# Performance work log

Measured on AMD Instinct MI355X. Metric: run time of the kernel, lower is better.

Reference implementation:

```python
import jax, jax.numpy as jnp
import numpy as np

D = 256
H = 8
DH = D // H
N = 100000
B = 256
T = 131072
HID_FUSE = 256   # fuse MLP hidden = d_model
HID_HEAD = 256   # QuantileHeads hidden
NQ = 3           # quantiles (q10, q50, q90)


def setup_inputs() -> dict:
    key = jax.random.key(0)
    ks = jax.random.split(key, 32)
    p = lambda k, *s: (0.02 * jax.random.normal(k, s, dtype=jnp.float32))
    inp = {
        'node_embeddings': jax.random.normal(ks[0], (N, D), dtype=jnp.float32),
        'target_index': jax.random.randint(ks[1], (B,), 0, N),
        'port_index': jax.random.randint(ks[2], (T,), 0, N),
        'port_batch': jnp.sort(jax.random.randint(ks[3], (T,), 0, B)),
        'port_weight': jax.random.uniform(ks[4], (T,), dtype=jnp.float32),
        # PMA pooling params (learnable seed + MHA projections, no biases)
        'seed': p(ks[5], D),
        'Wq_p': p(ks[6], D, D), 'Wk_p': p(ks[7], D, D), 'Wv_p': p(ks[8], D, D), 'Wo_p': p(ks[9], D, D),
        # target->portfolio cross-attention params
        'Wq_c': p(ks[10], D, D), 'Wk_c': p(ks[11], D, D), 'Wv_c': p(ks[12], D, D), 'Wo_c': p(ks[13], D, D),
        # fuse LayerNorm(3d) + MLP
        'ln_g': jnp.ones((3 * D,), jnp.float32), 'ln_b': jnp.zeros((3 * D,), jnp.float32),
        'fuse_W1': p(ks[14], 3 * D, HID_FUSE), 'fuse_b1': jnp.zeros((HID_FUSE,), jnp.float32),
        'fuse_W2': p(ks[15], HID_FUSE, D), 'fuse_b2': jnp.zeros((D,), jnp.float32),
        # quantile heads MLP
        'head_W1': p(ks[16], D, HID_HEAD), 'head_b1': jnp.zeros((HID_HEAD,), jnp.float32),
        'head_W2': p(ks[17], HID_HEAD, NQ), 'head_b2': jnp.zeros((NQ,), jnp.float32),
    }
    return inp


def _segment_attend(logits, v, seg, num_segments):
    # logits [T,H], v [T,H,DH], seg [T] -> pooled [num_segments, H, DH]
    m = jax.ops.segment_max(logits, seg, num_segments=num_segments)  # [B,H]
    e = jnp.exp(logits - m[seg])                                      # [T,H]
    s = jax.ops.segment_sum(e, seg, num_segments=num_segments)        # [B,H]
    p = e / (s[seg] + 1e-9)
    return jax.ops.segment_sum(p[..., None] * v, seg, num_segments=num_segments)


def reference(node_embeddings, target_index, port_index, port_batch, port_weight,
              seed, Wq_p, Wk_p, Wv_p, Wo_p, Wq_c, Wk_c, Wv_c, Wo_c,
              ln_g, ln_b, fuse_W1, fuse_b1, fuse_W2, fuse_b2,
              head_W1, head_b1, head_W2, head_b2):
    b = target_index.shape[0]
    scale = float(DH) ** -0.5
    tgt = node_embeddings[target_index]          # [B,D]
    tok = node_embeddings[port_index]            # [T,D]
    logw = jnp.log(port_weight + 1e-8)           # DV01 weighting as logit bias

    # --- PMA: learnable seed query pools DV01-weighted portfolio tokens ---
    q_p = (seed @ Wq_p).reshape(H, DH)
    k_p = (tok @ Wk_p).reshape(-1, H, DH)
    v_p = (tok @ Wv_p).reshape(-1, H, DH)
    lg_p = jnp.einsum('thd,hd->th', k_p, q_p) * scale + logw[:, None]
    pooled = _segment_attend(lg_p, v_p, port_batch, b).reshape(b, D)
    contexts = pooled @ Wo_p                     # [B,D]; zeros for empty portfolios

    # --- target -> portfolio cross-attention (residual) ---
    q_c = (tgt @ Wq_c).reshape(b, H, DH)
    k_c = (tok @ Wk_c).reshape(-1, H, DH)
    v_c = (tok @ Wv_c).reshape(-1, H, DH)
    lg_c = jnp.einsum('thd,thd->th', k_c, q_c[port_batch]) * scale + logw[:, None]
    att = _segment_attend(lg_c, v_c, port_batch, b).reshape(b, D)
    fused = tgt + att @ Wo_c                     # [B,D]; == tgt for empty portfolios

    # --- fuse: concat -> LN -> MLP ---
    z = jnp.concatenate([tgt, contexts, fused], axis=-1)  # [B,3D]
    mu = jnp.mean(z, axis=-1, keepdims=True)
    var = jnp.var(z, axis=-1, keepdims=True)
    z = (z - mu) * jax.lax.rsqrt(var + 1e-5) * ln_g + ln_b
    z = jax.nn.relu(z @ fuse_W1 + fuse_b1) @ fuse_W2 + fuse_b2  # [B,D]

    # --- quantile heads ---
    out = jax.nn.relu(z @ head_W1 + head_b1) @ head_W2 + head_b2  # [B,NQ]
    return out
```

## Files before the change

### kernel.cpp

```cpp
#include <hip/hip_runtime.h>
#include <hip/hip_bf16.h>

typedef __attribute__((ext_vector_type(8))) short short8;
typedef __attribute__((ext_vector_type(4))) float floatx4;

#define SCALE 0.17677669529663687f

__device__ __forceinline__ unsigned short f2bf(float f) {
  unsigned int x = __float_as_uint(f);
  x += 0x7fffu + ((x >> 16) & 1u);
  return (unsigned short)(x >> 16);
}
__device__ __forceinline__ float bf2f(unsigned short u) {
  return __uint_as_float(((unsigned int)u) << 16);
}

__device__ __forceinline__ short8 load_cvt8(const float* p) {
  floatx4 a = *(const floatx4*)p;
  floatx4 b = *(const floatx4*)(p + 4);
  short8 r;
  r[0] = (short)f2bf(a[0]); r[1] = (short)f2bf(a[1]);
  r[2] = (short)f2bf(a[2]); r[3] = (short)f2bf(a[3]);
  r[4] = (short)f2bf(b[0]); r[5] = (short)f2bf(b[1]);
  r[6] = (short)f2bf(b[2]); r[7] = (short)f2bf(b[3]);
  return r;
}

__device__ __forceinline__ void matvec256(const float* __restrict__ W,
                                          const float* act, float* outv,
                                          float* red4, int tid) {
  const int c4 = tid & 63, kg = tid >> 6, c0 = c4 * 4;
  floatx4 acc = (floatx4){0.f, 0.f, 0.f, 0.f};
  const float* Wp = W + (size_t)(kg * 64) * 256 + c0;
  const float* ap = act + kg * 64;
  #pragma unroll 8
  for (int k = 0; k < 64; ++k) {
    floatx4 wv = *(const floatx4*)(Wp + (size_t)k * 256);
    float a = ap[k];
    acc[0] += a * wv[0]; acc[1] += a * wv[1];
    acc[2] += a * wv[2]; acc[3] += a * wv[3];
  }
  *(floatx4*)(red4 + kg * 256 + c0) = acc;
  __syncthreads();
  outv[tid] = red4[tid] + red4[256 + tid] + red4[512 + tid] + red4[768 + tid];
  __syncthreads();
}

__global__ __launch_bounds__(256) void setup_kernel(
    const float* __restrict__ node,
    const int* __restrict__ tgt_idx,
    const int* __restrict__ port_batch,
    const float* __restrict__ seed,
    const float* __restrict__ Wq_p,
    const float* __restrict__ Wk_p,
    const float* __restrict__ Wq_c,
    const float* __restrict__ Wk_c,
    unsigned short* __restrict__ u_p_t,
    unsigned short* __restrict__ u_c_all,
    int* __restrict__ seg, int T, int B)
{
  __shared__ float act_l[256];
  __shared__ float q_l[256];
  __shared__ __align__(16) float red4[1024];
  const int tid = threadIdx.x;
  const int b = blockIdx.x;

  if (tid == 0 || (tid == 64 && b == B - 1)) {
    int key = (tid == 0) ? b : B;
    int lo = 0, hi = T;
    while (lo < hi) { int mid = (lo + hi) >> 1; if (port_batch[mid] < key) lo = mid + 1; else hi = mid; }
    seg[key] = lo;
  }

  act_l[tid] = node[(size_t)tgt_idx[b] * 256 + tid];
  __syncthreads();
  matvec256(Wq_c, act_l, q_l, red4, tid);

  {
    float hs[8];
    #pragma unroll
    for (int h = 0; h < 8; ++h) hs[h] = 0.f;
    #pragma unroll
    for (int c = 0; c < 32; ++c) {
      floatx4 wa = *(const floatx4*)(Wk_c + (size_t)tid * 256 + c * 8);
      floatx4 wb = *(const floatx4*)(Wk_c + (size_t)tid * 256 + c * 8 + 4);
      const int h = c >> 2;
      #pragma unroll
      for (int j = 0; j < 4; ++j) hs[h] += wa[j] * q_l[c * 8 + j];
      #pragma unroll
      for (int j = 0; j < 4; ++j) hs[h] += wb[j] * q_l[c * 8 + 4 + j];
    }
    #pragma unroll
    for (int h = 0; h < 8; ++h)
      u_c_all[(size_t)b * 2048 + h * 256 + tid] = f2bf(hs[h]);
  }

  if (b == 0) {
    __syncthreads();
    act_l[tid] = seed[tid];
    __syncthreads();
    matvec256(Wq_p, act_l, q_l, red4, tid);
    float hs[8];
    #pragma unroll
    for (int h = 0; h < 8; ++h) hs[h] = 0.f;
    #pragma unroll
    for (int c = 0; c < 32; ++c) {
      floatx4 wa = *(const floatx4*)(Wk_p + (size_t)tid * 256 + c * 8);
      floatx4 wb = *(const floatx4*)(Wk_p + (size_t)tid * 256 + c * 8 + 4);
      const int h = c >> 2;
      #pragma unroll
      for (int j = 0; j < 4; ++j) hs[h] += wa[j] * q_l[c * 8 + j];
      #pragma unroll
      for (int j = 0; j < 4; ++j) hs[h] += wb[j] * q_l[c * 8 + 4 + j];
    }
    #pragma unroll
    for (int h = 0; h < 8; ++h) u_p_t[h * 256 + tid] = f2bf(hs[h]);
  }
}

__global__ __launch_bounds__(256, 4) void attn_kernel(
    const float* __restrict__ node,
    const int* __restrict__ port_index,
    const float* __restrict__ port_weight,
    const unsigned short* __restrict__ u_p_t,
    const unsigned short* __restrict__ u_c_all,
    const int* __restrict__ seg,
    float* __restrict__ slabs, int T, int S)
{
  __shared__ __align__(16) unsigned short tok_lds[64 * 264];
  __shared__ __align__(16) unsigned short E_t[16 * 72];
  __shared__ float l_lds[16];

  const int tid  = threadIdx.x;
  const int s    = blockIdx.x;
  const int b    = blockIdx.y;
  const int lane = tid & 63;
  const int w    = tid >> 6;
  const int q    = lane >> 4;
  const int n    = lane & 15;

  if (tid < 16) l_lds[tid] = 0.f;

  short8 ufrag[8];
  const unsigned short* ubase = (n < 8) ? (u_p_t + n * 256)
                                        : (u_c_all + (size_t)b * 2048 + (n - 8) * 256);
  #pragma unroll
  for (int s8 = 0; s8 < 8; ++s8)
    ufrag[s8] = *(const short8*)(ubase + q * 8 + s8 * 32);

  const int start  = seg[b];
  const int end    = seg[b + 1];
  const int ntiles = (end - start + 63) >> 6;

  floatx4 sacc[4];
  #pragma unroll
  for (int nt = 0; nt < 4; ++nt) sacc[nt] = (floatx4){0.f, 0.f, 0.f, 0.f};

  short8 cur[8], nxt[8];
  float pwc[4], pwn[4];

  __syncthreads();

  if (s < ntiles) {
    int t = start + s * 64 + w * 16 + n; int tc = t < T ? t : T - 1;
    const float* rp = node + (size_t)port_index[tc] * 256 + q * 8;
    #pragma unroll
    for (int k = 0; k < 8; ++k) cur[k] = load_cvt8(rp + k * 32);
    #pragma unroll
    for (int r = 0; r < 4; ++r) { int tr = start + s * 64 + w * 16 + q * 4 + r; pwc[r] = port_weight[tr < T ? tr : T - 1]; }
  }

  for (int it = s; it < ntiles; it += S) {
    const int tbase = start + it * 64;
    if (it + S < ntiles) {
      int t = start + (it + S) * 64 + w * 16 + n; int tc = t < T ? t : T - 1;
      const float* rp = node + (size_t)port_index[tc] * 256 + q * 8;
      #pragma unroll
      for (int k = 0; k < 8; ++k) nxt[k] = load_cvt8(rp + k * 32);
      #pragma unroll
      for (int r = 0; r < 4; ++r) { int tr = start + (it + S) * 64 + w * 16 + q * 4 + r; pwn[r] = port_weight[tr < T ? tr : T - 1]; }
    }
    floatx4 lacc = (floatx4){0.f, 0.f, 0.f, 0.f};
    #pragma unroll
    for (int k = 0; k < 8; ++k)
      lacc = __builtin_amdgcn_mfma_f32_16x16x32_bf16(cur[k], ufrag[k], lacc, 0, 0, 0);
    float lsum = 0.f;
    #pragma unroll
    for (int r = 0; r < 4; ++r) {
      const int tr = tbase + w * 16 + q * 4 + r;
      float e = 0.f;
      if (tr < end) {
        float lg = lacc[r] * SCALE + logf(pwc[r] + 1e-8f);
        e = __expf(lg);
      }
      unsigned short eb = f2bf(e);
      E_t[n * 72 + w * 16 + q * 4 + r] = eb;
      lsum += bf2f(eb);
    }
    lsum += __shfl_xor(lsum, 16, 64);
    lsum += __shfl_xor(lsum, 32, 64);
    if (lane < 16) atomicAdd(&l_lds[lane], lsum);
    #pragma unroll
    for (int k = 0; k < 8; ++k)
      *(short8*)(tok_lds + (w * 16 + n) * 264 + q * 8 + k * 32) = cur[k];
    __syncthreads();
    short8 ea0 = *(const short8*)(E_t + n * 72 + q * 8);
    short8 ea1 = *(const short8*)(E_t + n * 72 + 32 + q * 8);
    #pragma unroll
    for (int nt = 0; nt < 4; ++nt) {
      const int dcol = w * 64 + nt * 16 + n;
      short8 b0, b1;
      #pragma unroll
      for (int j = 0; j < 8; ++j) b0[j] = (short)tok_lds[(q * 8 + j) * 264 + dcol];
      #pragma unroll
      for (int j = 0; j < 8; ++j) b1[j] = (short)tok_lds[(32 + q * 8 + j) * 264 + dcol];
      sacc[nt] = __builtin_amdgcn_mfma_f32_16x16x32_bf16(ea0, b0, sacc[nt], 0, 0, 0);
      sacc[nt] = __builtin_amdgcn_mfma_f32_16x16x32_bf16(ea1, b1, sacc[nt], 0, 0, 0);
    }
    __syncthreads();
    #pragma unroll
    for (int k = 0; k < 8; ++k) cur[k] = nxt[k];
    #pragma unroll
    for (int r = 0; r < 4; ++r) pwc[r] = pwn[r];
  }

  float* sl = slabs + ((size_t)b * S + s) * 4224;
  #pragma unroll
  for (int nt = 0; nt < 4; ++nt)
    #pragma unroll
    for (int r = 0; r < 4; ++r)
      sl[(q * 4 + r) * 256 + w * 64 + nt * 16 + n] = sacc[nt][r];
  if (tid < 16) sl[4096 + tid] = l_lds[tid];
}

__global__ __launch_bounds__(256) void k_slab_gemm(
    const float* __restrict__ slabs, int S,
    const float* __restrict__ Wv_p, const float* __restrict__ Wv_c,
    float* __restrict__ X)
{
  __shared__ float act_l[4 * 256];
  __shared__ float lsum[4];
  const int tid = threadIdx.x;
  const int bt = blockIdx.x, nt = blockIdx.y, z = blockIdx.z;
  const int head = nt >> 1;
  const int row = z * 8 + head;
  if (tid < 4) {
    const float* sl = slabs + (size_t)(bt * 4 + tid) * S * 4224;
    float l = 0.f;
    for (int s = 0; s < S; ++s) l += sl[s * 4224 + 4096 + row];
    lsum[tid] = 1.0f / (l + 1e-9f);
  }
  __syncthreads();
  for (int i = tid; i < 4 * 256; i += 256) {
    int m = i >> 8, k = i & 255;
    const float* sl = slabs + (size_t)(bt * 4 + m) * S * 4224;
    float sum = 0.f;
    for (int s = 0; s < S; ++s) sum += sl[s * 4224 + row * 256 + k];
    act_l[i] = sum * lsum[m];
  }
  __syncthreads();
  const int m = tid >> 6, lane = tid & 63, ks = lane >> 4, n = lane & 15;
  const int n0 = nt * 16;
  const float* W = z ? Wv_c : Wv_p;
  float acc = 0.f;
  const float* Wp = W + (size_t)(ks * 64) * 256 + n0 + n;
  const float* ap = &act_l[m * 256 + ks * 64];
  #pragma unroll 8
  for (int k = 0; k < 64; ++k) acc += ap[k] * Wp[(size_t)k * 256];
  acc += __shfl_xor(acc, 16, 64);
  acc += __shfl_xor(acc, 32, 64);
  if (ks == 0)
    X[(size_t)(bt * 4 + m) * 512 + z * 256 + n0 + n] = acc;
}

__global__ __launch_bounds__(256) void k_plain_gemm(
    const float* __restrict__ act, int act_ld,
    const float* __restrict__ W0, const float* __restrict__ W1,
    const float* __restrict__ bias0, const float* __restrict__ bias1,
    float* __restrict__ outp, int out_ld,
    int K, int relu)
{
  __shared__ float act_l[4 * 768];
  const int tid = threadIdx.x;
  const int bt = blockIdx.x, nt = blockIdx.y, z = blockIdx.z;
  const float* W = z ? W1 : W0;
  const float* bias = z ? bias1 : bias0;
  for (int i = tid; i < 4 * K; i += 256) {
    int m = i / K, k = i - m * K;
    act_l[m * K + k] = act[(size_t)(bt * 4 + m) * act_ld + z * K + k];
  }
  __syncthreads();
  const int m = tid >> 6, lane = tid & 63, ks = lane >> 4, n = lane & 15;
  const int n0 = nt * 16;
  const int Kq = K >> 2;
  float acc = 0.f;
  const float* Wp = W + (size_t)(ks * Kq) * 256 + n0 + n;
  const float* ap = &act_l[m * K + ks * Kq];
  #pragma unroll 8
  for (int k = 0; k < Kq; ++k) acc += ap[k] * Wp[(size_t)k * 256];
  acc += __shfl_xor(acc, 16, 64);
  acc += __shfl_xor(acc, 32, 64);
  if (ks == 0) {
    float v = acc + (bias ? bias[n0 + n] : 0.f);
    if (relu) v = fmaxf(v, 0.f);
    outp[(size_t)(bt * 4 + m) * out_ld + z * 256 + n0 + n] = v;
  }
}

__global__ __launch_bounds__(256) void k_ln_gemm(
    const float* __restrict__ node, const int* __restrict__ tgt_idx,
    const float* __restrict__ zbuf,
    const float* __restrict__ ln_g, const float* __restrict__ ln_b,
    const float* __restrict__ fuse_W1, const float* __restrict__ fuse_b1,
    float* __restrict__ h1)
{
  __shared__ float act_l[4 * 768];
  const int tid = threadIdx.x;
  const int bt = blockIdx.x, nt = blockIdx.y;
  for (int i = tid; i < 4 * 256; i += 256) {
    int m = i >> 8, k = i & 255;
    int b = bt * 4 + m;
    float tg = node[(size_t)tgt_idx[b] * 256 + k];
    float C  = zbuf[(size_t)b * 512 + k];
    float Fp = zbuf[(size_t)b * 512 + 256 + k];
    act_l[m * 768 + k]       = tg;
    act_l[m * 768 + 256 + k] = C;
    act_l[m * 768 + 512 + k] = tg + Fp;
  }
  __syncthreads();
  const int m = tid >> 6, lane = tid & 63;
  {
    float s = 0.f;
    for (int k = lane; k < 768; k += 64) s += act_l[m * 768 + k];
    #pragma unroll
    for (int o = 32; o >= 1; o >>= 1) s += __shfl_xor(s, o, 64);
    const float mu = s * (1.0f / 768.0f);
    float v = 0.f;
    for (int k = lane; k < 768; k += 64) { float d = act_l[m * 768 + k] - mu; v += d * d; }
    #pragma unroll
    for (int o = 32; o >= 1; o >>= 1) v += __shfl_xor(v, o, 64);
    const float rstd = 1.0f / sqrtf(v * (1.0f / 768.0f) + 1e-5f);
    for (int k = lane; k < 768; k += 64)
      act_l[m * 768 + k] = (act_l[m * 768 + k] - mu) * rstd * ln_g[k] + ln_b[k];
  }
  __syncthreads();
  const int ks = lane >> 4, n = lane & 15;
  const int n0 = nt * 16;
  float acc = 0.f;
  const float* Wp = fuse_W1 + (size_t)(ks * 192) * 256 + n0 + n;
  const float* ap = &act_l[m * 768 + ks * 192];
  #pragma unroll 8
  for (int k = 0; k < 192; ++k) acc += ap[k] * Wp[(size_t)k * 256];
  acc += __shfl_xor(acc, 16, 64);
  acc += __shfl_xor(acc, 32, 64);
  if (ks == 0)
    h1[(size_t)(bt * 4 + m) * 256 + n0 + n] = fmaxf(acc + fuse_b1[n0 + n], 0.f);
}

__global__ __launch_bounds__(256) void k_outhead(
    const float* __restrict__ hh, const float* __restrict__ head_W2,
    const float* __restrict__ head_b2, float* __restrict__ out)
{
  const int tid = threadIdx.x;
  const int m = tid >> 6, lane = tid & 63;
  const int b = blockIdx.x * 4 + m;
  float a0 = 0.f, a1 = 0.f, a2 = 0.f;
  for (int k = lane; k < 256; k += 64) {
    float h = hh[(size_t)b * 256 + k];
    a0 += h * head_W2[k * 3 + 0];
    a1 += h * head_W2[k * 3 + 1];
    a2 += h * head_W2[k * 3 + 2];
  }
  #pragma unroll
  for (int o = 32; o >= 1; o >>= 1) {
    a0 += __shfl_xor(a0, o, 64);
    a1 += __shfl_xor(a1, o, 64);
    a2 += __shfl_xor(a2, o, 64);
  }
  if (lane == 0) {
    out[b * 3 + 0] = a0 + head_b2[0];
    out[b * 3 + 1] = a1 + head_b2[1];
    out[b * 3 + 2] = a2 + head_b2[2];
  }
}

extern "C" void kernel_launch(void* const* d_in, const int* in_sizes, int n_in,
                              void* d_out, int out_size, void* d_ws, size_t ws_size,
                              hipStream_t stream) {
  const float* node        = (const float*)d_in[0];
  const int*   tgt_idx     = (const int*)d_in[1];
  const int*   port_index  = (const int*)d_in[2];
  const int*   port_batch  = (const int*)d_in[3];
  const float* port_weight = (const float*)d_in[4];
  const float* seed        = (const float*)d_in[5];
  const float* Wq_p = (const float*)d_in[6];
  const float* Wk_p = (const float*)d_in[7];
  const float* Wv_p = (const float*)d_in[8];
  const float* Wo_p = (const float*)d_in[9];
  const float* Wq_c = (const float*)d_in[10];
  const float* Wk_c = (const float*)d_in[11];
  const float* Wv_c = (const float*)d_in[12];
  const float* Wo_c = (const float*)d_in[13];
  const float* ln_g = (const float*)d_in[14];
  const float* ln_b = (const float*)d_in[15];
  const float* fuse_W1 = (const float*)d_in[16];
  const float* fuse_b1 = (const float*)d_in[17];
  const float* fuse_W2 = (const float*)d_in[18];
  const float* fuse_b2 = (const float*)d_in[19];
  const float* head_W1 = (const float*)d_in[20];
  const float* head_b1 = (const float*)d_in[21];
  const float* head_W2 = (const float*)d_in[22];
  const float* head_b2 = (const float*)d_in[23];

  const int B = in_sizes[1];
  const int T = in_sizes[2];

  char* ws = (char*)d_ws;
  unsigned short* u_p_t   = (unsigned short*)ws;
  int*            seg     = (int*)(ws + 4096);
  unsigned short* u_c_all = (unsigned short*)(ws + 8192);
  float* X    = (float*)(ws + 8192);
  float* zbuf = (float*)(ws + 8192 + (size_t)B * 2048);
  size_t slab_off = 8192 + (size_t)B * 4096;
  float* slabs = (float*)(ws + slab_off);
  float* h1 = slabs;
  float* z2 = h1 + (size_t)B * 256;
  float* hh = z2 + (size_t)B * 256;

  size_t per_slice = (size_t)B * 4224 * 4;
  int S = 1;
  if (ws_size > slab_off) {
    size_t fit = (ws_size - slab_off) / per_slice;
    S = (int)(fit < 1 ? 1 : (fit > 8 ? 8 : fit));
  }

  const int BT = B / 4;

  setup_kernel<<<B, 256, 0, stream>>>(node, tgt_idx, port_batch, seed,
      Wq_p, Wk_p, Wq_c, Wk_c, u_p_t, u_c_all, seg, T, B);
  attn_kernel<<<dim3(S, B), 256, 0, stream>>>(node, port_index, port_weight,
      u_p_t, u_c_all, seg, slabs, T, S);
  k_slab_gemm<<<dim3(BT, 16, 2), 256, 0, stream>>>(slabs, S, Wv_p, Wv_c, X);
  k_plain_gemm<<<dim3(BT, 16, 2), 256, 0, stream>>>(X, 512, Wo_p, Wo_c,
      nullptr, nullptr, zbuf, 512, 256, 0);
  k_ln_gemm<<<dim3(BT, 16), 256, 0, stream>>>(node, tgt_idx, zbuf,
      ln_g, ln_b, fuse_W1, fuse_b1, h1);
  k_plain_gemm<<<dim3(BT, 16, 1), 256, 0, stream>>>(h1, 256, fuse_W2, nullptr,
      fuse_b2, nullptr, z2, 256, 256, 0);
  k_plain_gemm<<<dim3(BT, 16, 1), 256, 0, stream>>>(z2, 256, head_W1, nullptr,
      head_b1, nullptr, hh, 256, 256, 1);
  k_outhead<<<BT, 256, 0, stream>>>(hh, head_W2, head_b2, (float*)d_out);
}
```

Before: 359.8 us.

## Drop register prefetch, stage slab stores through LDS, reduce split count

Removes the software-pipelined next-tile register prefetch in the attention kernel and loads each tile's gathered rows inside the loop. This cuts register pressure, and the launch bound drops from 4 to 2 blocks per CU. The partial-sum output is now staged through LDS so the slab write uses coalesced 16-byte stores. The split count S is capped at 4 instead of 8, which shrinks the slab reduction work but leaves fewer blocks to hide gather latency.

```diff
diff --git a/kernel.cpp b/kernel.cpp
--- a/kernel.cpp
+++ b/kernel.cpp
@@ -118,7 +118,7 @@
   }
 }
 
-__global__ __launch_bounds__(256, 4) void attn_kernel(
+__global__ __launch_bounds__(256, 2) void attn_kernel(
     const float* __restrict__ node,
     const int* __restrict__ port_index,
     const float* __restrict__ port_weight,
@@ -156,30 +156,21 @@
   #pragma unroll
   for (int nt = 0; nt < 4; ++nt) sacc[nt] = (floatx4){0.f, 0.f, 0.f, 0.f};
 
-  short8 cur[8], nxt[8];
-  float pwc[4], pwn[4];
-
-  __syncthreads();
-
-  if (s < ntiles) {
-    int t = start + s * 64 + w * 16 + n; int tc = t < T ? t : T - 1;
-    const float* rp = node + (size_t)port_index[tc] * 256 + q * 8;
-    #pragma unroll
-    for (int k = 0; k < 8; ++k) cur[k] = load_cvt8(rp + k * 32);
-    #pragma unroll
-    for (int r = 0; r < 4; ++r) { int tr = start + s * 64 + w * 16 + q * 4 + r; pwc[r] = port_weight[tr < T ? tr : T - 1]; }
-  }
+  __syncthreads();
 
   for (int it = s; it < ntiles; it += S) {
     const int tbase = start + it * 64;
-    if (it + S < ntiles) {
-      int t = start + (it + S) * 64 + w * 16 + n; int tc = t < T ? t : T - 1;
+    short8 cur[8];
+    {
+      int t = tbase + w * 16 + n; int tc = t < T ? t : T - 1;
       const float* rp = node + (size_t)port_index[tc] * 256 + q * 8;
       #pragma unroll
-      for (int k = 0; k < 8; ++k) nxt[k] = load_cvt8(rp + k * 32);
-      #pragma unroll
-      for (int r = 0; r < 4; ++r) { int tr = start + (it + S) * 64 + w * 16 + q * 4 + r; pwn[r] = port_weight[tr < T ? tr : T - 1]; }
+      for (int k = 0; k < 8; ++k) cur[k] = load_cvt8(rp + k * 32);
     }
+    float pw[4];
+    #pragma unroll
+    for (int r = 0; r < 4; ++r) { int tr = tbase + w * 16 + q * 4 + r; pw[r] = port_weight[tr < T ? tr : T - 1]; }
+
     floatx4 lacc = (floatx4){0.f, 0.f, 0.f, 0.f};
     #pragma unroll
     for (int k = 0; k < 8; ++k)
@@ -190,7 +181,7 @@
       const int tr = tbase + w * 16 + q * 4 + r;
       float e = 0.f;
       if (tr < end) {
-        float lg = lacc[r] * SCALE + logf(pwc[r] + 1e-8f);
+        float lg = lacc[r] * SCALE + logf(pw[r] + 1e-8f);
         e = __expf(lg);
       }
       unsigned short eb = f2bf(e);
@@ -218,18 +209,22 @@
       sacc[nt] = __builtin_amdgcn_mfma_f32_16x16x32_bf16(ea1, b1, sacc[nt], 0, 0, 0);
     }
     __syncthreads();
-    #pragma unroll
-    for (int k = 0; k < 8; ++k) cur[k] = nxt[k];
-    #pragma unroll
-    for (int r = 0; r < 4; ++r) pwc[r] = pwn[r];
-  }
-
+  }
+
+  float* stage = (float*)tok_lds;
+  #pragma unroll
+  for (int nt = 0; nt < 4; ++nt)
+    #pragma unroll
+    for (int r = 0; r < 4; ++r)
+      stage[(q * 4 + r) * 256 + w * 64 + nt * 16 + n] = sacc[nt][r];
+  __syncthreads();
   float* sl = slabs + ((size_t)b * S + s) * 4224;
   #pragma unroll
-  for (int nt = 0; nt < 4; ++nt)
-    #pragma unroll
-    for (int r = 0; r < 4; ++r)
-      sl[(q * 4 + r) * 256 + w * 64 + nt * 16 + n] = sacc[nt][r];
+  for (int i = 0; i < 4; ++i) {
+    const int row = i * 4 + w;
+    const int c0 = (tid & 63) * 4;
+    *(floatx4*)(sl + row * 256 + c0) = *(const floatx4*)(stage + row * 256 + c0);
+  }
   if (tid < 16) sl[4096 + tid] = l_lds[tid];
 }
 
@@ -431,7 +426,7 @@
   int S = 1;
   if (ws_size > slab_off) {
     size_t fit = (ws_size - slab_off) / per_slice;
-    S = (int)(fit < 1 ? 1 : (fit > 8 ? 8 : fit));
+    S = (int)(fit < 1 ? 1 : (fit > 4 ? 4 : fit));
   }
 
   const int BT = B / 4;
```

Result: faster. 319.6 us (-11.2%).
